# Kernel optimization log

Hardware: AMD Instinct MI355X
Metric: run time of the kernel (lower is better)

The kernel has to match this reference:

```python
import jax, jax.numpy as jnp
import numpy as np

N = 4096
IN_DIM = 512
OUT_DIM = 64
NUM_HEADS = 8
DENSITY = 0.01  # adjacency density


def setup_inputs() -> dict:
    key = jax.random.key(0)
    ks = jax.random.split(key, 9)
    h = jax.random.normal(ks[0], (N, IN_DIM), dtype=jnp.float32)
    # sparse adjacency realized as a dense 0/1 mask (the module calls A.to_dense())
    A = (jax.random.uniform(ks[1], (N, N)) < DENSITY).astype(jnp.float32)
    s_in = 1.0 / np.sqrt(IN_DIM)
    Wq = jax.random.normal(ks[2], (IN_DIM, OUT_DIM * NUM_HEADS), dtype=jnp.float32) * s_in
    bq = jax.random.normal(ks[3], (OUT_DIM * NUM_HEADS,), dtype=jnp.float32) * s_in
    Wk = jax.random.normal(ks[4], (IN_DIM, OUT_DIM * NUM_HEADS), dtype=jnp.float32) * s_in
    bk = jax.random.normal(ks[5], (OUT_DIM * NUM_HEADS,), dtype=jnp.float32) * s_in
    Wv = jax.random.normal(ks[6], (IN_DIM, OUT_DIM * NUM_HEADS), dtype=jnp.float32) * s_in
    bv = jax.random.normal(ks[7], (OUT_DIM * NUM_HEADS,), dtype=jnp.float32) * s_in
    return {"A": A, "h": h, "Wq": Wq, "bq": bq, "Wk": Wk, "bk": bk, "Wv": Wv, "bv": bv}


def reference(A, h, Wq, bq, Wk, bk, Wv, bv):
    n = h.shape[0]
    scaling = OUT_DIM ** (-0.5)
    # (N, out_dim, H) to match torch .reshape(N, out_dim, num_heads)
    q = ((h @ Wq) + bq).reshape(n, OUT_DIM, NUM_HEADS) * scaling
    k = ((h @ Wk) + bk).reshape(n, OUT_DIM, NUM_HEADS)
    v = ((h @ Wv) + bv).reshape(n, OUT_DIM, NUM_HEADS)
    # attn[h,n,m] = sum_d q[n,d,h] * k[m,d,h], masked by dense adjacency
    attn = jnp.einsum('ndh,mdh->hnm', q, k) * A[None, :, :]
    # NOTE: original code softmaxes over dim=0 == the HEAD axis (faithful)
    attn = jax.nn.softmax(attn, axis=0)
    # out[h,n,d] = sum_m attn[h,n,m] * v[m,d,h]
    out = jnp.einsum('hnm,mdh->hnd', attn, v)
    # raw row-major reshape of (H, N, D) -> (N, H*D), as in the original
    return out.reshape(n, -1)
```

## Files before the change

kernel.cpp:

```cpp
#include <hip/hip_runtime.h>

typedef unsigned short u16;
typedef unsigned short u16x8 __attribute__((ext_vector_type(8)));
typedef __bf16 bf16x8 __attribute__((ext_vector_type(8)));
typedef float f32x4 __attribute__((ext_vector_type(4)));

#define NN 4096
#define KD 512
#define HD 512
#define NT 1536

__device__ __forceinline__ u16 f2bf(float f) {
    unsigned u = __builtin_bit_cast(unsigned, f);
    u += 0x7fffu + ((u >> 16) & 1u);
    return (u16)(u >> 16);
}
__device__ __forceinline__ float bf2f(u16 u) {
    return __builtin_bit_cast(float, ((unsigned)u) << 16);
}

__global__ void k_cvt_h(const float4* __restrict__ in, u16* __restrict__ out) {
    int i = blockIdx.x * blockDim.x + threadIdx.x;
    float4 f = in[i];
    ((ushort4*)out)[i] = make_ushort4(f2bf(f.x), f2bf(f.y), f2bf(f.z), f2bf(f.w));
}

__global__ void k_w(const float* __restrict__ Wq, const float* __restrict__ Wk,
                    const float* __restrict__ Wv, u16* __restrict__ wt) {
    __shared__ float tile[32][33];
    int z = blockIdx.z;
    const float* W = (z == 0) ? Wq : ((z == 1) ? Wk : Wv);
    float scale = (z == 0) ? 0.125f : 1.0f;
    int j0 = blockIdx.x * 32;
    int k0 = blockIdx.y * 32;
    int tx = threadIdx.x, ty = threadIdx.y;
    #pragma unroll
    for (int r = 0; r < 32; r += 8)
        tile[ty + r][tx] = W[(size_t)(k0 + ty + r) * HD + j0 + tx];
    __syncthreads();
    #pragma unroll
    for (int r = 0; r < 32; r += 8)
        wt[(size_t)(z * 512 + j0 + ty + r) * KD + k0 + tx] = f2bf(scale * tile[tx][ty + r]);
}

__global__ void k_bias(const float* __restrict__ bq, const float* __restrict__ bk,
                       const float* __restrict__ bv, float* __restrict__ biasf) {
    int t = threadIdx.x, b = blockIdx.x;
    float v = (b == 0) ? bq[t] * 0.125f : ((b == 1) ? bk[t] : bv[t]);
    biasf[b * 512 + t] = v;
}

__global__ __launch_bounds__(256) void k_gemm(const u16* __restrict__ hb,
        const u16* __restrict__ wt, const float* __restrict__ biasf,
        float* __restrict__ qbuf, u16* __restrict__ kbuf, u16* __restrict__ vbuf)
{
    __shared__ u16 As[128 * 32];
    __shared__ u16 Bs[128 * 32];
    const int tid = threadIdx.x;
    const int w = tid >> 6, lane = tid & 63;
    const int wr = w >> 1, wc = w & 1;
    const int l16 = lane & 15, half = lane >> 4;
    const int row0 = blockIdx.x * 128, col0 = blockIdx.y * 128;

    const int crow = tid >> 2, c8 = (tid & 3) * 8;
    const u16* gA0 = hb + (size_t)(row0 + crow) * KD + c8;
    const u16* gA1 = gA0 + (size_t)64 * KD;
    const u16* gB0 = wt + (size_t)(col0 + crow) * KD + c8;
    const u16* gB1 = gB0 + (size_t)64 * KD;

    f32x4 acc[4][4] = {};

    for (int kk = 0; kk < KD; kk += 32) {
        u16x8 a0 = *(const u16x8*)(gA0 + kk);
        u16x8 a1 = *(const u16x8*)(gA1 + kk);
        u16x8 b0 = *(const u16x8*)(gB0 + kk);
        u16x8 b1 = *(const u16x8*)(gB1 + kk);
        __syncthreads();
        *(u16x8*)&As[tid * 8] = a0;
        *(u16x8*)&As[(tid + 256) * 8] = a1;
        *(u16x8*)&Bs[tid * 8] = b0;
        *(u16x8*)&Bs[(tid + 256) * 8] = b1;
        __syncthreads();
        bf16x8 af[4], bfr[4];
        #pragma unroll
        for (int mi = 0; mi < 4; ++mi)
            af[mi] = *(const bf16x8*)&As[(wr * 64 + mi * 16 + l16) * 32 + half * 8];
        #pragma unroll
        for (int ni = 0; ni < 4; ++ni)
            bfr[ni] = *(const bf16x8*)&Bs[(wc * 64 + ni * 16 + l16) * 32 + half * 8];
        #pragma unroll
        for (int mi = 0; mi < 4; ++mi)
            #pragma unroll
            for (int ni = 0; ni < 4; ++ni)
                acc[mi][ni] = __builtin_amdgcn_mfma_f32_16x16x32_bf16(
                    af[mi], bfr[ni], acc[mi][ni], 0, 0, 0);
    }

    #pragma unroll
    for (int mi = 0; mi < 4; ++mi) {
        #pragma unroll
        for (int ni = 0; ni < 4; ++ni) {
            int j = col0 + wc * 64 + ni * 16 + l16;
            float bj = biasf[j];
            #pragma unroll
            for (int r = 0; r < 4; ++r) {
                int m = row0 + wr * 64 + mi * 16 + half * 4 + r;
                float val = acc[mi][ni][r] + bj;
                if (j < 512)       qbuf[(size_t)m * 512 + j] = val;
                else if (j < 1024) kbuf[(size_t)m * 512 + (j - 512)] = f2bf(val);
                else               vbuf[(size_t)m * 512 + (j - 1024)] = f2bf(val);
            }
        }
    }
}

__global__ void k_colsum(const u16* __restrict__ vbuf, float* __restrict__ colsum) {
    int t = threadIdx.x;
    int b = blockIdx.x;
    float acc = 0.f;
    const u16* p = vbuf + (size_t)b * 64 * 512 + t;
    #pragma unroll 4
    for (int r = 0; r < 64; ++r) acc += bf2f(p[r * 512]);
    atomicAdd(&colsum[t], acc);
}

__global__ __launch_bounds__(256) void k_attn(const float* __restrict__ A,
        const float* __restrict__ qbuf, const u16* __restrict__ kbuf,
        const u16* __restrict__ vbuf, const float* __restrict__ colsum,
        float* __restrict__ out)
{
    const int n = blockIdx.x, tid = threadIdx.x;
    const int w = tid >> 6, lane = tid & 63;
    __shared__ float s_q[512], s_out[512];
    __shared__ int s_idx[1024];
    __shared__ int s_cnt;
    if (tid == 0) s_cnt = 0;
    s_q[tid]        = qbuf[(size_t)n * 512 + tid];
    s_q[tid + 256]  = qbuf[(size_t)n * 512 + 256 + tid];
    s_out[tid]       = 0.125f * colsum[tid];
    s_out[tid + 256] = 0.125f * colsum[tid + 256];
    __syncthreads();

    const float4* arow = (const float4*)(A + (size_t)n * NN);
    for (int c4 = tid; c4 < NN / 4; c4 += 256) {
        float4 a = arow[c4];
        int m0 = c4 * 4;
        if (a.x != 0.f) s_idx[atomicAdd(&s_cnt, 1)] = m0;
        if (a.y != 0.f) s_idx[atomicAdd(&s_cnt, 1)] = m0 + 1;
        if (a.z != 0.f) s_idx[atomicAdd(&s_cnt, 1)] = m0 + 2;
        if (a.w != 0.f) s_idx[atomicAdd(&s_cnt, 1)] = m0 + 3;
    }
    __syncthreads();
    const int cnt = s_cnt;

    float acc[8] = {0.f, 0.f, 0.f, 0.f, 0.f, 0.f, 0.f, 0.f};
    for (int i = w; i < cnt; i += 4) {
        const int m = s_idx[i];
        const u16* kr = kbuf + (size_t)m * 512;
        float s = 0.f;
        #pragma unroll
        for (int j = 0; j < 8; ++j)
            s += s_q[lane + 64 * j] * bf2f(kr[lane + 64 * j]);
        s += __shfl_xor(s, 8);
        s += __shfl_xor(s, 16);
        s += __shfl_xor(s, 32);
        float mx = s;
        mx = fmaxf(mx, __shfl_xor(mx, 1));
        mx = fmaxf(mx, __shfl_xor(mx, 2));
        mx = fmaxf(mx, __shfl_xor(mx, 4));
        float e = __expf(s - mx);
        float Z = e;
        Z += __shfl_xor(Z, 1);
        Z += __shfl_xor(Z, 2);
        Z += __shfl_xor(Z, 4);
        const float c = e / Z - 0.125f;
        const u16* vr = vbuf + (size_t)m * 512;
        #pragma unroll
        for (int j = 0; j < 8; ++j)
            acc[j] += c * bf2f(vr[lane + 64 * j]);
    }

    for (int sel = 0; sel < 4; ++sel) {
        if (w == sel) {
            #pragma unroll
            for (int j = 0; j < 8; ++j)
                s_out[lane + 64 * j] += acc[j];
        }
        __syncthreads();
    }

    for (int i2 = tid; i2 < 512; i2 += 256) {
        int hh = i2 >> 6, d = i2 & 63;
        out[(size_t)hh * (NN * 64) + (size_t)n * 64 + d] = s_out[d * 8 + hh];
    }
}

extern "C" void kernel_launch(void* const* d_in, const int* in_sizes, int n_in,
                              void* d_out, int out_size, void* d_ws, size_t ws_size,
                              hipStream_t stream)
{
    const float* A  = (const float*)d_in[0];
    const float* h  = (const float*)d_in[1];
    const float* Wq = (const float*)d_in[2];
    const float* bq = (const float*)d_in[3];
    const float* Wk = (const float*)d_in[4];
    const float* bk = (const float*)d_in[5];
    const float* Wv = (const float*)d_in[6];
    const float* bv = (const float*)d_in[7];
    float* out = (float*)d_out;

    char* ws = (char*)d_ws;
    float* qbuf   = (float*)(ws);
    u16*   kbuf   = (u16*)(ws + (8u  << 20));
    u16*   vbuf   = (u16*)(ws + (12u << 20));
    u16*   hb     = (u16*)(ws + (16u << 20));
    u16*   wt     = (u16*)(ws + (20u << 20));
    float* biasf  = (float*)(ws + (22u << 20));
    float* colsum = (float*)(ws + (22u << 20) + 8192);

    k_cvt_h<<<dim3(2048), dim3(256), 0, stream>>>((const float4*)h, hb);
    k_w<<<dim3(16, 16, 3), dim3(32, 8), 0, stream>>>(Wq, Wk, Wv, wt);
    k_bias<<<dim3(3), dim3(512), 0, stream>>>(bq, bk, bv, biasf);
    k_gemm<<<dim3(32, 12), dim3(256), 0, stream>>>(hb, wt, biasf, qbuf, kbuf, vbuf);
    hipMemsetAsync(colsum, 0, 512 * sizeof(float), stream);
    k_colsum<<<dim3(64), dim3(512), 0, stream>>>(vbuf, colsum);
    k_attn<<<dim3(4096), dim3(256), 0, stream>>>(A, qbuf, kbuf, vbuf, colsum, out);
}
```

Baseline: 173.7 us.

## Permute head layout, async LDS GEMM loads, separate edge extraction kernel

Permutes the projection output columns so each lane's head-dimension elements are contiguous, which lets the attention kernel use 16-byte vector loads of q, k and v. The GEMM switches to direct global-to-LDS loads with an XOR-swizzled, 64-wide K tile. Edge index extraction moves from the attention kernel into a separate grid-stride kernel that fills per-row neighbor lists with global atomics. Rows are capped at 128 neighbors, which risks dropping edges, and the hb workspace region is reused for cnt and idx after the GEMM has consumed it.

Result: slower. 241.8 us (+39.2%).

```diff
diff --git a/kernel.cpp b/kernel.cpp
--- a/kernel.cpp
+++ b/kernel.cpp
@@ -8,7 +8,6 @@
 #define NN 4096
 #define KD 512
 #define HD 512
-#define NT 1536
 
 __device__ __forceinline__ u16 f2bf(float f) {
     unsigned u = __builtin_bit_cast(unsigned, f);
@@ -18,6 +17,11 @@
 __device__ __forceinline__ float bf2f(u16 u) {
     return __builtin_bit_cast(float, ((unsigned)u) << 16);
 }
+__device__ __forceinline__ int permj(int j) { return ((j & 7) << 6) | (j >> 3); }
+
+#define GLOAD16(gp, lp) \
+    __builtin_amdgcn_global_load_lds((const __attribute__((address_space(1))) void*)(gp), \
+                                     (__attribute__((address_space(3))) void*)(lp), 16, 0, 0)
 
 __global__ void k_cvt_h(const float4* __restrict__ in, u16* __restrict__ out) {
     int i = blockIdx.x * blockDim.x + threadIdx.x;
@@ -31,85 +35,117 @@
     int z = blockIdx.z;
     const float* W = (z == 0) ? Wq : ((z == 1) ? Wk : Wv);
     float scale = (z == 0) ? 0.125f : 1.0f;
-    int j0 = blockIdx.x * 32;
-    int k0 = blockIdx.y * 32;
+    int j0 = blockIdx.x * 32, k0 = blockIdx.y * 32;
     int tx = threadIdx.x, ty = threadIdx.y;
     #pragma unroll
     for (int r = 0; r < 32; r += 8)
         tile[ty + r][tx] = W[(size_t)(k0 + ty + r) * HD + j0 + tx];
     __syncthreads();
     #pragma unroll
-    for (int r = 0; r < 32; r += 8)
-        wt[(size_t)(z * 512 + j0 + ty + r) * KD + k0 + tx] = f2bf(scale * tile[tx][ty + r]);
+    for (int r = 0; r < 32; r += 8) {
+        int j = j0 + ty + r;
+        wt[(size_t)(z * 512 + permj(j)) * KD + k0 + tx] = f2bf(scale * tile[tx][ty + r]);
+    }
 }
 
 __global__ void k_bias(const float* __restrict__ bq, const float* __restrict__ bk,
-                       const float* __restrict__ bv, float* __restrict__ biasf) {
+                       const float* __restrict__ bv, float* __restrict__ pbias) {
     int t = threadIdx.x, b = blockIdx.x;
     float v = (b == 0) ? bq[t] * 0.125f : ((b == 1) ? bk[t] : bv[t]);
-    biasf[b * 512 + t] = v;
+    pbias[b * 512 + permj(t)] = v;
 }
 
 __global__ __launch_bounds__(256) void k_gemm(const u16* __restrict__ hb,
-        const u16* __restrict__ wt, const float* __restrict__ biasf,
+        const u16* __restrict__ wt, const float* __restrict__ pbias,
         float* __restrict__ qbuf, u16* __restrict__ kbuf, u16* __restrict__ vbuf)
 {
-    __shared__ u16 As[128 * 32];
-    __shared__ u16 Bs[128 * 32];
+    __shared__ u16 As[128 * 64];
+    __shared__ u16 Bs[128 * 64];
     const int tid = threadIdx.x;
     const int w = tid >> 6, lane = tid & 63;
     const int wr = w >> 1, wc = w & 1;
     const int l16 = lane & 15, half = lane >> 4;
     const int row0 = blockIdx.x * 128, col0 = blockIdx.y * 128;
-
-    const int crow = tid >> 2, c8 = (tid & 3) * 8;
-    const u16* gA0 = hb + (size_t)(row0 + crow) * KD + c8;
-    const u16* gA1 = gA0 + (size_t)64 * KD;
-    const u16* gB0 = wt + (size_t)(col0 + crow) * KD + c8;
-    const u16* gB1 = gB0 + (size_t)64 * KD;
+    const int la = lane & 7, lb = lane >> 3;
+    const int swcol = ((la ^ lb) << 3);
+
+    const u16* gA[4]; const u16* gB[4];
+    u16* lA[4]; u16* lB[4];
+    #pragma unroll
+    for (int s = 0; s < 4; ++s) {
+        int i = w * 4 + s;
+        gA[s] = hb + (size_t)(row0 + 8 * i + lb) * KD + swcol;
+        gB[s] = wt + (size_t)(col0 + 8 * i + lb) * KD + swcol;
+        lA[s] = As + i * 512;
+        lB[s] = Bs + i * 512;
+    }
 
     f32x4 acc[4][4] = {};
 
-    for (int kk = 0; kk < KD; kk += 32) {
-        u16x8 a0 = *(const u16x8*)(gA0 + kk);
-        u16x8 a1 = *(const u16x8*)(gA1 + kk);
-        u16x8 b0 = *(const u16x8*)(gB0 + kk);
-        u16x8 b1 = *(const u16x8*)(gB1 + kk);
+    for (int kk = 0; kk < KD; kk += 64) {
+        #pragma unroll
+        for (int s = 0; s < 4; ++s) {
+            GLOAD16(gA[s] + kk, lA[s]);
+            GLOAD16(gB[s] + kk, lB[s]);
+        }
         __syncthreads();
-        *(u16x8*)&As[tid * 8] = a0;
-        *(u16x8*)&As[(tid + 256) * 8] = a1;
-        *(u16x8*)&Bs[tid * 8] = b0;
-        *(u16x8*)&Bs[(tid + 256) * 8] = b1;
+        #pragma unroll
+        for (int kk2 = 0; kk2 < 2; ++kk2) {
+            bf16x8 af[4], bf[4];
+            #pragma unroll
+            for (int mi = 0; mi < 4; ++mi) {
+                int row = wr * 64 + mi * 16 + l16;
+                int off = row * 128 + (((kk2 << 6) | (half << 4)) ^ ((l16 & 7) << 4));
+                af[mi] = *(const bf16x8*)((const char*)As + off);
+            }
+            #pragma unroll
+            for (int ni = 0; ni < 4; ++ni) {
+                int row = wc * 64 + ni * 16 + l16;
+                int off = row * 128 + (((kk2 << 6) | (half << 4)) ^ ((l16 & 7) << 4));
+                bf[ni] = *(const bf16x8*)((const char*)Bs + off);
+            }
+            #pragma unroll
+            for (int mi = 0; mi < 4; ++mi)
+                #pragma unroll
+                for (int ni = 0; ni < 4; ++ni)
+                    acc[mi][ni] = __builtin_amdgcn_mfma_f32_16x16x32_bf16(
+                        af[mi], bf[ni], acc[mi][ni], 0, 0, 0);
+        }
         __syncthreads();
-        bf16x8 af[4], bfr[4];
+    }
+
+    const int seg = blockIdx.y >> 2;
+    #pragma unroll
+    for (int ni = 0; ni < 4; ++ni) {
+        int j = col0 + wc * 64 + ni * 16 + l16;
+        float bj = pbias[j];
         #pragma unroll
-        for (int mi = 0; mi < 4; ++mi)
-            af[mi] = *(const bf16x8*)&As[(wr * 64 + mi * 16 + l16) * 32 + half * 8];
-        #pragma unroll
-        for (int ni = 0; ni < 4; ++ni)
-            bfr[ni] = *(const bf16x8*)&Bs[(wc * 64 + ni * 16 + l16) * 32 + half * 8];
-        #pragma unroll
-        for (int mi = 0; mi < 4; ++mi)
-            #pragma unroll
-            for (int ni = 0; ni < 4; ++ni)
-                acc[mi][ni] = __builtin_amdgcn_mfma_f32_16x16x32_bf16(
-                    af[mi], bfr[ni], acc[mi][ni], 0, 0, 0);
-    }
-
-    #pragma unroll
-    for (int mi = 0; mi < 4; ++mi) {
-        #pragma unroll
-        for (int ni = 0; ni < 4; ++ni) {
-            int j = col0 + wc * 64 + ni * 16 + l16;
-            float bj = biasf[j];
+        for (int mi = 0; mi < 4; ++mi) {
             #pragma unroll
             for (int r = 0; r < 4; ++r) {
                 int m = row0 + wr * 64 + mi * 16 + half * 4 + r;
                 float val = acc[mi][ni][r] + bj;
-                if (j < 512)       qbuf[(size_t)m * 512 + j] = val;
-                else if (j < 1024) kbuf[(size_t)m * 512 + (j - 512)] = f2bf(val);
+                if (seg == 0)      qbuf[(size_t)m * 512 + j] = val;
+                else if (seg == 1) kbuf[(size_t)m * 512 + (j - 512)] = f2bf(val);
                 else               vbuf[(size_t)m * 512 + (j - 1024)] = f2bf(val);
             }
+        }
+    }
+}
+
+__global__ __launch_bounds__(256) void k_edges(const float4* __restrict__ A4,
+        int* __restrict__ cnt, int* __restrict__ idx) {
+    int t = blockIdx.x * blockDim.x + threadIdx.x;
+    int stride = gridDim.x * blockDim.x;
+    for (int i = t; i < NN * NN / 4; i += stride) {
+        float4 a = A4[i];
+        if (a.x != 0.f || a.y != 0.f || a.z != 0.f || a.w != 0.f) {
+            int n = i >> 10;
+            int m0 = (i & 1023) * 4;
+            if (a.x != 0.f) { int p = atomicAdd(&cnt[n], 1); if (p < 128) idx[n * 128 + p] = m0; }
+            if (a.y != 0.f) { int p = atomicAdd(&cnt[n], 1); if (p < 128) idx[n * 128 + p] = m0 + 1; }
+            if (a.z != 0.f) { int p = atomicAdd(&cnt[n], 1); if (p < 128) idx[n * 128 + p] = m0 + 2; }
+            if (a.w != 0.f) { int p = atomicAdd(&cnt[n], 1); if (p < 128) idx[n * 128 + p] = m0 + 3; }
         }
     }
 }
@@ -124,74 +160,56 @@
     atomicAdd(&colsum[t], acc);
 }
 
-__global__ __launch_bounds__(256) void k_attn(const float* __restrict__ A,
-        const float* __restrict__ qbuf, const u16* __restrict__ kbuf,
-        const u16* __restrict__ vbuf, const float* __restrict__ colsum,
-        float* __restrict__ out)
+__global__ __launch_bounds__(256) void k_attn(const int* __restrict__ cnt,
+        const int* __restrict__ idx, const float* __restrict__ qbuf,
+        const u16* __restrict__ kbuf, const u16* __restrict__ vbuf,
+        const float* __restrict__ colsum, float* __restrict__ out)
 {
     const int n = blockIdx.x, tid = threadIdx.x;
     const int w = tid >> 6, lane = tid & 63;
-    __shared__ float s_q[512], s_out[512];
-    __shared__ int s_idx[1024];
-    __shared__ int s_cnt;
-    if (tid == 0) s_cnt = 0;
-    s_q[tid]        = qbuf[(size_t)n * 512 + tid];
-    s_q[tid + 256]  = qbuf[(size_t)n * 512 + 256 + tid];
-    s_out[tid]       = 0.125f * colsum[tid];
-    s_out[tid + 256] = 0.125f * colsum[tid + 256];
+    __shared__ float s_out[512];
+    s_out[tid] = 0.f;
+    s_out[tid + 256] = 0.f;
+
+    const float4 qa = *(const float4*)(qbuf + (size_t)n * 512 + lane * 8);
+    const float4 qb = *(const float4*)(qbuf + (size_t)n * 512 + lane * 8 + 4);
+    int c = cnt[n];
+    if (c > 128) c = 128;
     __syncthreads();
 
-    const float4* arow = (const float4*)(A + (size_t)n * NN);
-    for (int c4 = tid; c4 < NN / 4; c4 += 256) {
-        float4 a = arow[c4];
-        int m0 = c4 * 4;
-        if (a.x != 0.f) s_idx[atomicAdd(&s_cnt, 1)] = m0;
-        if (a.y != 0.f) s_idx[atomicAdd(&s_cnt, 1)] = m0 + 1;
-        if (a.z != 0.f) s_idx[atomicAdd(&s_cnt, 1)] = m0 + 2;
-        if (a.w != 0.f) s_idx[atomicAdd(&s_cnt, 1)] = m0 + 3;
-    }
-    __syncthreads();
-    const int cnt = s_cnt;
-
     float acc[8] = {0.f, 0.f, 0.f, 0.f, 0.f, 0.f, 0.f, 0.f};
-    for (int i = w; i < cnt; i += 4) {
-        const int m = s_idx[i];
-        const u16* kr = kbuf + (size_t)m * 512;
-        float s = 0.f;
-        #pragma unroll
-        for (int j = 0; j < 8; ++j)
-            s += s_q[lane + 64 * j] * bf2f(kr[lane + 64 * j]);
-        s += __shfl_xor(s, 8);
-        s += __shfl_xor(s, 16);
-        s += __shfl_xor(s, 32);
-        float mx = s;
-        mx = fmaxf(mx, __shfl_xor(mx, 1));
-        mx = fmaxf(mx, __shfl_xor(mx, 2));
-        mx = fmaxf(mx, __shfl_xor(mx, 4));
+    for (int i = w; i < c; i += 4) {
+        const int m = idx[n * 128 + i];
+        u16x8 kv = *(const u16x8*)(kbuf + (size_t)m * 512 + lane * 8);
+        float s = qa.x * bf2f(kv[0]) + qa.y * bf2f(kv[1]) + qa.z * bf2f(kv[2]) + qa.w * bf2f(kv[3])
+                + qb.x * bf2f(kv[4]) + qb.y * bf2f(kv[5]) + qb.z * bf2f(kv[6]) + qb.w * bf2f(kv[7]);
+        s += __shfl_xor(s, 1);
+        s += __shfl_xor(s, 2);
+        s += __shfl_xor(s, 4);
+        float mx = fmaxf(s, __shfl_xor(s, 8));
+        mx = fmaxf(mx, __shfl_xor(mx, 16));
+        mx = fmaxf(mx, __shfl_xor(mx, 32));
         float e = __expf(s - mx);
         float Z = e;
-        Z += __shfl_xor(Z, 1);
-        Z += __shfl_xor(Z, 2);
-        Z += __shfl_xor(Z, 4);
-        const float c = e / Z - 0.125f;
-        const u16* vr = vbuf + (size_t)m * 512;
-        #pragma unroll
-        for (int j = 0; j < 8; ++j)
-            acc[j] += c * bf2f(vr[lane + 64 * j]);
-    }
-
-    for (int sel = 0; sel < 4; ++sel) {
-        if (w == sel) {
-            #pragma unroll
-            for (int j = 0; j < 8; ++j)
-                s_out[lane + 64 * j] += acc[j];
-        }
-        __syncthreads();
-    }
+        Z += __shfl_xor(Z, 8);
+        Z += __shfl_xor(Z, 16);
+        Z += __shfl_xor(Z, 32);
+        const float cc = e / Z - 0.125f;
+        u16x8 vv = *(const u16x8*)(vbuf + (size_t)m * 512 + lane * 8);
+        acc[0] += cc * bf2f(vv[0]); acc[1] += cc * bf2f(vv[1]);
+        acc[2] += cc * bf2f(vv[2]); acc[3] += cc * bf2f(vv[3]);
+        acc[4] += cc * bf2f(vv[4]); acc[5] += cc * bf2f(vv[5]);
+        acc[6] += cc * bf2f(vv[6]); acc[7] += cc * bf2f(vv[7]);
+    }
+
+    #pragma unroll
+    for (int j = 0; j < 8; ++j)
+        atomicAdd(&s_out[lane * 8 + j], acc[j]);
+    __syncthreads();
 
     for (int i2 = tid; i2 < 512; i2 += 256) {
         int hh = i2 >> 6, d = i2 & 63;
-        out[(size_t)hh * (NN * 64) + (size_t)n * 64 + d] = s_out[d * 8 + hh];
+        out[(size_t)hh * (NN * 64) + (size_t)n * 64 + d] = s_out[i2] + 0.125f * colsum[i2];
     }
 }
 
@@ -215,14 +233,18 @@
     u16*   vbuf   = (u16*)(ws + (12u << 20));
     u16*   hb     = (u16*)(ws + (16u << 20));
     u16*   wt     = (u16*)(ws + (20u << 20));
-    float* biasf  = (float*)(ws + (22u << 20));
-    float* colsum = (float*)(ws + (22u << 20) + 8192);
+    float* pbias  = (float*)(ws + (21u << 20) + (512u << 10));
+    int*   cnt    = (int*)(ws + (16u << 20));
+    int*   idx    = (int*)(ws + (16u << 20) + (64u << 10));
+    float* colsum = (float*)(ws + (19u << 20));
 
     k_cvt_h<<<dim3(2048), dim3(256), 0, stream>>>((const float4*)h, hb);
     k_w<<<dim3(16, 16, 3), dim3(32, 8), 0, stream>>>(Wq, Wk, Wv, wt);
-    k_bias<<<dim3(3), dim3(512), 0, stream>>>(bq, bk, bv, biasf);
-    k_gemm<<<dim3(32, 12), dim3(256), 0, stream>>>(hb, wt, biasf, qbuf, kbuf, vbuf);
+    k_bias<<<dim3(3), dim3(512), 0, stream>>>(bq, bk, bv, pbias);
+    k_gemm<<<dim3(32, 12), dim3(256), 0, stream>>>(hb, wt, pbias, qbuf, kbuf, vbuf);
+    hipMemsetAsync(cnt, 0, 4096 * sizeof(int), stream);
     hipMemsetAsync(colsum, 0, 512 * sizeof(float), stream);
+    k_edges<<<dim3(2048), dim3(256), 0, stream>>>((const float4*)A, cnt, idx);
     k_colsum<<<dim3(64), dim3(512), 0, stream>>>(vbuf, colsum);
-    k_attn<<<dim3(4096), dim3(256), 0, stream>>>(A, qbuf, kbuf, vbuf, colsum, out);
-}
+    k_attn<<<dim3(4096), dim3(256), 0, stream>>>(cnt, idx, qbuf, kbuf, vbuf, colsum, out);
+}
```
